# Kernel optimization log

Hardware: AMD Instinct MI355X
Metric: run time of the kernel (lower is better)

The kernel has to match this reference:

```python
import jax, jax.numpy as jnp
import numpy as np

EPS = 1e-5
GROUPS = 32
N_HEADS = 8
HEAD_DIM = 64


def setup_inputs() -> dict:
    key = jax.random.key(0)
    ks = jax.random.split(key, 8)
    b, c, d, w, hs = 2, 512, 16, 16, 16
    ctx_len, ctx_dim = 1024, 768
    inner = N_HEADS * HEAD_DIM  # 512
    return {
        "x": jax.random.normal(ks[0], (b, c, d, w, hs), jnp.float32),
        "context": jax.random.normal(ks[1], (b, ctx_len, ctx_dim), jnp.float32),
        "gamma": jnp.ones((c,), jnp.float32),
        "beta": jnp.zeros((c,), jnp.float32),
        "Wq": jax.random.normal(ks[2], (c, inner), jnp.float32) * (c ** -0.5),
        "Wk": jax.random.normal(ks[3], (ctx_dim, inner), jnp.float32) * (ctx_dim ** -0.5),
        "Wv": jax.random.normal(ks[4], (ctx_dim, inner), jnp.float32) * (ctx_dim ** -0.5),
        "Wo": jax.random.normal(ks[5], (inner, c), jnp.float32) * (inner ** -0.5),
        "bo": jnp.zeros((c,), jnp.float32),
    }


def reference(x, context, gamma, beta, Wq, Wk, Wv, Wo, bo):
    b, c, d, w, hs = x.shape
    n = d * w * hs  # sequence length of voxel tokens
    scale = HEAD_DIM ** -0.5

    # GroupNorm over (channels-in-group, spatial)
    xg = x.reshape(b, GROUPS, -1)
    mu = jnp.mean(xg, axis=-1, keepdims=True)
    var = jnp.mean(jnp.square(xg - mu), axis=-1, keepdims=True)
    xn = (xg - mu) * jax.lax.rsqrt(var + EPS)
    xn = xn.reshape(b, c, n) * gamma[None, :, None] + beta[None, :, None]

    x_seq = jnp.swapaxes(x.reshape(b, c, n), 1, 2)   # [b, n, c] residual
    xn_seq = jnp.swapaxes(xn, 1, 2)                   # [b, n, c]

    q = (xn_seq @ Wq).reshape(b, n, N_HEADS, HEAD_DIM)
    k = (context @ Wk).reshape(b, -1, N_HEADS, HEAD_DIM)
    v = (context @ Wv).reshape(b, -1, N_HEADS, HEAD_DIM)

    attn = jax.nn.softmax(jnp.einsum('bqhd,bkhd->bhqk', q, k) * scale, axis=-1)
    out = jnp.einsum('bhqk,bkhd->bqhd', attn, v).reshape(b, n, N_HEADS * HEAD_DIM)

    out = out @ Wo + bo  # dropout is identity in eval mode
    out = out + x_seq
    return jnp.swapaxes(out, 1, 2).reshape(b, c, d, w, hs)
```

## Files before the change

### kernel.cpp

```cpp
#include <hip/hip_runtime.h>
#include <hip/hip_bf16.h>

#define B 2
#define C 512
#define NTOK 4096
#define GROUPS 32
#define CPG 16
#define CTX 1024
#define CDIM 768
#define NH 8
#define HD 64
#define INNER 512
#define EPS 1e-5f
#define KVBLK 64
#define NCH (CTX / KVBLK)
#define LOG2E 1.44269504f

typedef unsigned short bf16_t;
typedef __attribute__((ext_vector_type(8))) short bf16x8;
typedef __attribute__((ext_vector_type(4))) float f32x4;

__device__ __forceinline__ bf16_t f2b(float f) {
    unsigned u = __float_as_uint(f);
    u += 0x7fffu + ((u >> 16) & 1u);
    return (bf16_t)(u >> 16);
}

__device__ __forceinline__ float4 pack8(const float* v) {
    union { ushort s[8]; float4 f; } u;
    #pragma unroll
    for (int j = 0; j < 8; ++j) u.s[j] = f2b(v[j]);
    return u.f;
}

__device__ __forceinline__ int swz(int row, int col) {
    return row * 64 + (col ^ ((row & 7) << 3));
}

__global__ __launch_bounds__(256) void gn_partial_kernel(const float* __restrict__ x,
                                                         float2* __restrict__ partials) {
    int blk = blockIdx.x;
    const float* base = x + (size_t)blk * 4096;
    float s = 0.f, ss = 0.f;
    #pragma unroll
    for (int i = 0; i < 4; ++i) {
        float4 v = *(const float4*)&base[(threadIdx.x + i * 256) * 4];
        s += v.x + v.y + v.z + v.w;
        ss += v.x * v.x + v.y * v.y + v.z * v.z + v.w * v.w;
    }
    #pragma unroll
    for (int o = 32; o > 0; o >>= 1) { s += __shfl_xor(s, o); ss += __shfl_xor(ss, o); }
    __shared__ float ls[2][4];
    int wv = threadIdx.x >> 6, ln = threadIdx.x & 63;
    if (ln == 0) { ls[0][wv] = s; ls[1][wv] = ss; }
    __syncthreads();
    if (threadIdx.x == 0) {
        partials[blk] = make_float2(ls[0][0] + ls[0][1] + ls[0][2] + ls[0][3],
                                    ls[1][0] + ls[1][1] + ls[1][2] + ls[1][3]);
    }
}

__global__ __launch_bounds__(256) void gn_apply_kernel(const float* __restrict__ x,
                                                       const float2* __restrict__ partials,
                                                       const float* __restrict__ gamma,
                                                       const float* __restrict__ beta,
                                                       bf16_t* __restrict__ xn) {
    __shared__ float tile[32][33];
    __shared__ float gmu[2], grs[2];
    int b = blockIdx.z;
    int c0 = blockIdx.y * 32;
    int t0 = blockIdx.x * 32;
    int tid = threadIdx.x;
    if (tid < 32) {
        int gi = tid >> 4, pi = tid & 15;
        float2 pp = partials[b * C + c0 + gi * 16 + pi];
        float s = pp.x, ss = pp.y;
        #pragma unroll
        for (int o = 8; o > 0; o >>= 1) { s += __shfl_xor(s, o); ss += __shfl_xor(ss, o); }
        if (pi == 0) {
            float mu = s / (float)(CPG * NTOK);
            float var = ss / (float)(CPG * NTOK) - mu * mu;
            gmu[gi] = mu;
            grs[gi] = rsqrtf(var + EPS);
        }
    }
    int tt = tid & 31, cr = tid >> 5;
    __syncthreads();
    #pragma unroll
    for (int i = 0; i < 4; ++i) {
        int co = cr + 8 * i;
        int c = c0 + co;
        float mu = gmu[co >> 4], rs = grs[co >> 4];
        float v = x[((size_t)(b * C + c)) * NTOK + t0 + tt];
        tile[co][tt] = (v - mu) * rs * gamma[c] + beta[c];
    }
    __syncthreads();
    #pragma unroll
    for (int i = 0; i < 4; ++i) {
        int t = t0 + cr + 8 * i;
        int c = c0 + tt;
        xn[((size_t)b * NTOK + t) * C + c] = f2b(tile[tt][cr + 8 * i]);
    }
}

__global__ __launch_bounds__(256) void wcast_all_kernel(
    const float* __restrict__ Wq, const float* __restrict__ Wk,
    const float* __restrict__ Wv, const float* __restrict__ Wo,
    bf16_t* __restrict__ Wqt, bf16_t* __restrict__ Wkvt, bf16_t* __restrict__ Wot) {
    int z = blockIdx.z;
    const float* in; bf16_t* out; int K;
    if (z == 0)      { in = Wq; out = Wqt;  K = C; }
    else if (z == 1) { in = Wk; out = Wkvt; K = CDIM; }
    else if (z == 2) { in = Wv; out = Wkvt + (size_t)INNER * CDIM; K = CDIM; }
    else             { in = Wo; out = Wot;  K = INNER; }
    int k0 = blockIdx.x * 32, n0 = blockIdx.y * 32;
    if (k0 >= K) return;
    __shared__ float t[32][33];
    int xx = threadIdx.x & 31, yy = threadIdx.x >> 5;
    #pragma unroll
    for (int i = 0; i < 4; ++i)
        t[yy + 8 * i][xx] = in[(size_t)(k0 + yy + 8 * i) * INNER + n0 + xx];
    __syncthreads();
    #pragma unroll
    for (int i = 0; i < 4; ++i)
        out[(size_t)(n0 + yy + 8 * i) * K + k0 + xx] = f2b(t[xx][yy + 8 * i]);
}

template <int AFP32>
__global__ __launch_bounds__(256) void gemm_qkv_kernel(
    const void* __restrict__ Av, const bf16_t* __restrict__ Bt,
    bf16_t* __restrict__ outK, bf16_t* __restrict__ outV,
    int K, int seqshift, float oscale, int vtrans) {
    __shared__ __align__(16) bf16_t As[64][40];
    __shared__ __align__(16) bf16_t Bs[64][40];
    const int tid = threadIdx.x;
    const int l = tid & 63, w = tid >> 6;
    const int wr = w >> 1, wc = w & 1;
    const int lg = l >> 4, lr = l & 15;
    const int m0 = blockIdx.x * 64, n0 = blockIdx.y * 64;
    const int rowS = tid >> 2, c8 = (tid & 3) * 8;
    const bf16_t* pa16 = AFP32 ? nullptr : (const bf16_t*)Av + (size_t)(m0 + rowS) * K + c8;
    const float*  pa32 = AFP32 ? (const float*)Av + (size_t)(m0 + rowS) * K + c8 : nullptr;
    const bf16_t* pb = Bt + (size_t)(n0 + rowS) * K + c8;
    f32x4 acc[2][2] = {};
    float av[8];
    float4 ra, rb;
    if (AFP32) {
        *(float4*)&av[0] = *(const float4*)pa32;
        *(float4*)&av[4] = *(const float4*)(pa32 + 4);
        ra = pack8(av);
    } else {
        ra = *(const float4*)pa16;
    }
    rb = *(const float4*)pb;
    *(float4*)&As[rowS][c8] = ra;
    *(float4*)&Bs[rowS][c8] = rb;
    for (int k0 = 0; k0 < K; k0 += 32) {
        __syncthreads();
        if (k0 + 32 < K) {
            if (AFP32) {
                *(float4*)&av[0] = *(const float4*)(pa32 + k0 + 32);
                *(float4*)&av[4] = *(const float4*)(pa32 + k0 + 36);
                ra = pack8(av);
            } else {
                ra = *(const float4*)(pa16 + k0 + 32);
            }
            rb = *(const float4*)(pb + k0 + 32);
        }
        bf16x8 af[2], bfm[2];
        af[0]  = *(bf16x8*)&As[wr * 32 + lr][lg * 8];
        af[1]  = *(bf16x8*)&As[wr * 32 + 16 + lr][lg * 8];
        bfm[0] = *(bf16x8*)&Bs[wc * 32 + lr][lg * 8];
        bfm[1] = *(bf16x8*)&Bs[wc * 32 + 16 + lr][lg * 8];
        #pragma unroll
        for (int mi = 0; mi < 2; ++mi)
            #pragma unroll
            for (int ni = 0; ni < 2; ++ni)
                acc[mi][ni] = __builtin_amdgcn_mfma_f32_16x16x32_bf16(af[mi], bfm[ni], acc[mi][ni], 0, 0, 0);
        __syncthreads();
        if (k0 + 32 < K) {
            *(float4*)&As[rowS][c8] = ra;
            *(float4*)&Bs[rowS][c8] = rb;
        }
    }
    const int seqmask = (1 << seqshift) - 1;
    #pragma unroll
    for (int ni = 0; ni < 2; ++ni) {
        int n = n0 + wc * 32 + ni * 16 + lr;
        int nn = n & (INNER - 1);
        int h = nn >> 6, dd = nn & 63;
        bool isV = (n >= INNER);
        #pragma unroll
        for (int mi = 0; mi < 2; ++mi) {
            int mb = m0 + wr * 32 + mi * 16 + lg * 4;
            int bidx = mb >> seqshift, seqb = mb & seqmask;
            if (isV && vtrans) {
                ushort4 pv;
                pv.x = f2b(acc[mi][ni][0] * oscale);
                pv.y = f2b(acc[mi][ni][1] * oscale);
                pv.z = f2b(acc[mi][ni][2] * oscale);
                pv.w = f2b(acc[mi][ni][3] * oscale);
                *(ushort4*)&outV[((size_t)(bidx * NH + h) * HD + dd) * (size_t)(seqmask + 1) + seqb] = pv;
            } else {
                bf16_t* dst = isV ? outV : outK;
                #pragma unroll
                for (int r = 0; r < 4; ++r)
                    dst[(((size_t)(bidx * NH + h) << seqshift) + seqb + r) * HD + dd] =
                        f2b(acc[mi][ni][r] * oscale);
            }
        }
    }
}

__global__ __launch_bounds__(256) void gemm_o_kernel(
    const bf16_t* __restrict__ A, const bf16_t* __restrict__ Bt,
    const float* __restrict__ bo, const float* __restrict__ x,
    float* __restrict__ out) {
    __shared__ __align__(16) bf16_t As[64][40];
    __shared__ __align__(16) bf16_t Bs[64][40];
    const int tid = threadIdx.x;
    const int l = tid & 63, w = tid >> 6;
    const int wr = w >> 1, wc = w & 1;
    const int lg = l >> 4, lr = l & 15;
    const int m0 = blockIdx.x * 64, n0 = blockIdx.y * 64;
    const int rowS = tid >> 2, c8 = (tid & 3) * 8;
    const bf16_t* pa = A  + (size_t)(m0 + rowS) * INNER + c8;
    const bf16_t* pb = Bt + (size_t)(n0 + rowS) * INNER + c8;
    f32x4 acc[2][2] = {};
    float4 ra = *(const float4*)pa;
    float4 rb = *(const float4*)pb;
    *(float4*)&As[rowS][c8] = ra;
    *(float4*)&Bs[rowS][c8] = rb;
    for (int k0 = 0; k0 < INNER; k0 += 32) {
        __syncthreads();
        if (k0 + 32 < INNER) {
            ra = *(const float4*)(pa + k0 + 32);
            rb = *(const float4*)(pb + k0 + 32);
        }
        bf16x8 af[2], bfm[2];
        af[0]  = *(bf16x8*)&As[wr * 32 + lr][lg * 8];
        af[1]  = *(bf16x8*)&As[wr * 32 + 16 + lr][lg * 8];
        bfm[0] = *(bf16x8*)&Bs[wc * 32 + lr][lg * 8];
        bfm[1] = *(bf16x8*)&Bs[wc * 32 + 16 + lr][lg * 8];
        #pragma unroll
        for (int mi = 0; mi < 2; ++mi)
            #pragma unroll
            for (int ni = 0; ni < 2; ++ni)
                acc[mi][ni] = __builtin_amdgcn_mfma_f32_16x16x32_bf16(af[mi], bfm[ni], acc[mi][ni], 0, 0, 0);
        __syncthreads();
        if (k0 + 32 < INNER) {
            *(float4*)&As[rowS][c8] = ra;
            *(float4*)&Bs[rowS][c8] = rb;
        }
    }
    #pragma unroll
    for (int mi = 0; mi < 2; ++mi) {
        int mb = m0 + wr * 32 + mi * 16 + lg * 4;
        int t = mb & (NTOK - 1);
        int bb = mb >> 12;
        #pragma unroll
        for (int ni = 0; ni < 2; ++ni) {
            int cc = n0 + wc * 32 + ni * 16 + lr;
            size_t o = (((size_t)(bb * C + cc)) << 12) + t;
            float4 xr = *(const float4*)&x[o];
            float bias = bo[cc];
            float4 ov;
            ov.x = acc[mi][ni][0] + bias + xr.x;
            ov.y = acc[mi][ni][1] + bias + xr.y;
            ov.z = acc[mi][ni][2] + bias + xr.z;
            ov.w = acc[mi][ni][3] + bias + xr.w;
            *(float4*)&out[o] = ov;
        }
    }
}

__global__ __launch_bounds__(256) void attn_kernel(
    const bf16_t* __restrict__ Q, const bf16_t* __restrict__ Kb,
    const bf16_t* __restrict__ Vt, bf16_t* __restrict__ AO) {
    __shared__ __align__(16) bf16_t Ks[64 * 64];
    __shared__ __align__(16) bf16_t Vs[64 * 64];
    __shared__ __align__(16) bf16_t Ps[4][16 * 64];
    const int tid = threadIdx.x;
    const int l = tid & 63, w = tid >> 6;
    const int lg = l >> 4, lr = l & 15;
    const int bh = blockIdx.x >> 6;
    const int tile = blockIdx.x & 63;
    const int b = bh >> 3, h = bh & 7;
    const int t0 = tile * 64 + w * 16;

    const bf16_t* qbase = Q + ((size_t)bh * NTOK + t0 + lr) * HD;
    bf16x8 qf[2];
    qf[0] = *(const bf16x8*)&qbase[lg * 8];
    qf[1] = *(const bf16x8*)&qbase[32 + lg * 8];

    f32x4 acc[4] = {};
    float mrow[4], lrow[4];
    #pragma unroll
    for (int r = 0; r < 4; ++r) { mrow[r] = -1e30f; lrow[r] = 0.f; }

    const bf16_t* kbase = Kb + (size_t)bh * CTX * HD;
    const bf16_t* vbase = Vt + (size_t)bh * HD * CTX;
    const int srow = tid >> 3, sc8 = (tid & 7) * 8;

    float4 kr0 = *(const float4*)&kbase[(size_t)srow * HD + sc8];
    float4 kr1 = *(const float4*)&kbase[(size_t)(srow + 32) * HD + sc8];
    float4 vr0 = *(const float4*)&vbase[(size_t)srow * CTX + sc8];
    float4 vr1 = *(const float4*)&vbase[(size_t)(srow + 32) * CTX + sc8];
    *(float4*)&Ks[swz(srow, sc8)] = kr0;
    *(float4*)&Ks[swz(srow + 32, sc8)] = kr1;
    *(float4*)&Vs[swz(srow, sc8)] = vr0;
    *(float4*)&Vs[swz(srow + 32, sc8)] = vr1;

    for (int c = 0; c < NCH; ++c) {
        __syncthreads();
        if (c + 1 < NCH) {
            int k1 = (c + 1) * KVBLK;
            kr0 = *(const float4*)&kbase[(size_t)(k1 + srow) * HD + sc8];
            kr1 = *(const float4*)&kbase[(size_t)(k1 + srow + 32) * HD + sc8];
            vr0 = *(const float4*)&vbase[(size_t)srow * CTX + k1 + sc8];
            vr1 = *(const float4*)&vbase[(size_t)(srow + 32) * CTX + k1 + sc8];
        }
        f32x4 sf[4] = {};
        #pragma unroll
        for (int ks = 0; ks < 2; ++ks)
            #pragma unroll
            for (int ni = 0; ni < 4; ++ni) {
                bf16x8 kf = *(bf16x8*)&Ks[swz(ni * 16 + lr, ks * 32 + lg * 8)];
                sf[ni] = __builtin_amdgcn_mfma_f32_16x16x32_bf16(qf[ks], kf, sf[ni], 0, 0, 0);
            }
        #pragma unroll
        for (int r = 0; r < 4; ++r) {
            float s0 = sf[0][r], s1 = sf[1][r];
            float s2 = sf[2][r], s3 = sf[3][r];
            float cm = fmaxf(fmaxf(s0, s1), fmaxf(s2, s3));
            cm = fmaxf(cm, __shfl_xor(cm, 1));
            cm = fmaxf(cm, __shfl_xor(cm, 2));
            cm = fmaxf(cm, __shfl_xor(cm, 4));
            cm = fmaxf(cm, __shfl_xor(cm, 8));
            float mn = fmaxf(mrow[r], cm);
            float scl = __builtin_amdgcn_exp2f(mrow[r] - mn);
            float p0 = __builtin_amdgcn_exp2f(s0 - mn);
            float p1 = __builtin_amdgcn_exp2f(s1 - mn);
            float p2 = __builtin_amdgcn_exp2f(s2 - mn);
            float p3 = __builtin_amdgcn_exp2f(s3 - mn);
            float rs = p0 + p1 + p2 + p3;
            rs += __shfl_xor(rs, 1); rs += __shfl_xor(rs, 2);
            rs += __shfl_xor(rs, 4); rs += __shfl_xor(rs, 8);
            lrow[r] = lrow[r] * scl + rs;
            mrow[r] = mn;
            #pragma unroll
            for (int ni = 0; ni < 4; ++ni) acc[ni][r] *= scl;
            int prow = lg * 4 + r;
            Ps[w][swz(prow, 0 * 16 + lr)] = f2b(p0);
            Ps[w][swz(prow, 1 * 16 + lr)] = f2b(p1);
            Ps[w][swz(prow, 2 * 16 + lr)] = f2b(p2);
            Ps[w][swz(prow, 3 * 16 + lr)] = f2b(p3);
        }
        #pragma unroll
        for (int ks = 0; ks < 2; ++ks) {
            bf16x8 pf = *(bf16x8*)&Ps[w][swz(lr, ks * 32 + lg * 8)];
            #pragma unroll
            for (int ni = 0; ni < 4; ++ni) {
                bf16x8 vf = *(bf16x8*)&Vs[swz(ni * 16 + lr, ks * 32 + lg * 8)];
                acc[ni] = __builtin_amdgcn_mfma_f32_16x16x32_bf16(pf, vf, acc[ni], 0, 0, 0);
            }
        }
        __syncthreads();
        if (c + 1 < NCH) {
            *(float4*)&Ks[swz(srow, sc8)] = kr0;
            *(float4*)&Ks[swz(srow + 32, sc8)] = kr1;
            *(float4*)&Vs[swz(srow, sc8)] = vr0;
            *(float4*)&Vs[swz(srow + 32, sc8)] = vr1;
        }
    }

    #pragma unroll
    for (int ni = 0; ni < 4; ++ni)
        #pragma unroll
        for (int r = 0; r < 4; ++r) {
            int t = t0 + lg * 4 + r;
            AO[((size_t)b * NTOK + t) * INNER + h * HD + ni * 16 + lr] =
                f2b(acc[ni][r] / lrow[r]);
        }
}

extern "C" void kernel_launch(void* const* d_in, const int* in_sizes, int n_in,
                              void* d_out, int out_size, void* d_ws, size_t ws_size,
                              hipStream_t stream) {
    const float* x       = (const float*)d_in[0];
    const float* context = (const float*)d_in[1];
    const float* gamma   = (const float*)d_in[2];
    const float* beta    = (const float*)d_in[3];
    const float* Wq      = (const float*)d_in[4];
    const float* Wk      = (const float*)d_in[5];
    const float* Wv      = (const float*)d_in[6];
    const float* Wo      = (const float*)d_in[7];
    const float* bo      = (const float*)d_in[8];
    float* out = (float*)d_out;

    char* p = (char*)d_ws;
    float2* parts = (float2*)p;          p += 1024 * sizeof(float2);
    bf16_t* xn   = (bf16_t*)p;           p += (size_t)B * NTOK * C * 2;
    bf16_t* Wqt  = (bf16_t*)p;           p += (size_t)INNER * C * 2;
    bf16_t* Wkvt = (bf16_t*)p;           p += (size_t)2 * INNER * CDIM * 2;
    bf16_t* Wot  = (bf16_t*)p;           p += (size_t)C * INNER * 2;
    bf16_t* qb   = (bf16_t*)p;           p += (size_t)B * NH * NTOK * HD * 2;
    bf16_t* kb   = (bf16_t*)p;           p += (size_t)B * NH * CTX * HD * 2;
    bf16_t* vb   = (bf16_t*)p;           p += (size_t)B * NH * CTX * HD * 2;
    bf16_t* ao   = (bf16_t*)p;           p += (size_t)B * NTOK * INNER * 2;

    hipLaunchKernelGGL(gn_partial_kernel, dim3(B * C), dim3(256), 0, stream, x, parts);
    hipLaunchKernelGGL(gn_apply_kernel, dim3(NTOK / 32, C / 32, B), dim3(256), 0, stream,
                       x, parts, gamma, beta, xn);
    hipLaunchKernelGGL(wcast_all_kernel, dim3(24, 16, 4), dim3(256), 0, stream,
                       Wq, Wk, Wv, Wo, Wqt, Wkvt, Wot);
    hipLaunchKernelGGL((gemm_qkv_kernel<0>), dim3(128, 8), dim3(256), 0, stream,
                       (const void*)xn, Wqt, qb, qb, C, 12, 0.125f * LOG2E, 0);
    hipLaunchKernelGGL((gemm_qkv_kernel<1>), dim3(32, 16), dim3(256), 0, stream,
                       (const void*)context, Wkvt, kb, vb, CDIM, 10, 1.0f, 1);
    hipLaunchKernelGGL(attn_kernel, dim3(B * NH * (NTOK / 64)), dim3(256), 0, stream,
                       qb, kb, vb, ao);
    hipLaunchKernelGGL(gemm_o_kernel, dim3(128, 8), dim3(256), 0, stream,
                       ao, Wot, bo, x, out);
}
```

Baseline: 194.7 us.

## Transpose QK^T MFMA so each lane owns one query row in softmax

Swaps the MFMA operands for the score computation so the result is S^T, with each lane holding 16 scores of a single query row. The row max and row sum then need only two cross-lane shuffles instead of four per row times four rows, and running max/sum become scalars per lane. P is packed with v_cvt_pk_bf16_f32 and written to LDS as 8-byte stores instead of scalar 2-byte stores. The rescale factors and final denominators are redistributed to the accumulator layout with __shfl, which adds some shuffle traffic and relies on the inline-asm conversion being available on the target.

```diff
diff --git a/kernel.cpp b/kernel.cpp
--- a/kernel.cpp
+++ b/kernel.cpp
@@ -31,6 +31,12 @@
     #pragma unroll
     for (int j = 0; j < 8; ++j) u.s[j] = f2b(v[j]);
     return u.f;
+}
+
+__device__ __forceinline__ unsigned cvtpk(float lo, float hi) {
+    unsigned r;
+    asm("v_cvt_pk_bf16_f32 %0, %1, %2" : "=v"(r) : "v"(lo), "v"(hi));
+    return r;
 }
 
 __device__ __forceinline__ int swz(int row, int col) {
@@ -294,9 +300,8 @@
     qf[1] = *(const bf16x8*)&qbase[32 + lg * 8];
 
     f32x4 acc[4] = {};
-    float mrow[4], lrow[4];
-    #pragma unroll
-    for (int r = 0; r < 4; ++r) { mrow[r] = -1e30f; lrow[r] = 0.f; }
+    float mrow = -1e30f;
+    float lrow = 0.f;
 
     const bf16_t* kbase = Kb + (size_t)bh * CTX * HD;
     const bf16_t* vbase = Vt + (size_t)bh * HD * CTX;
@@ -326,39 +331,47 @@
             #pragma unroll
             for (int ni = 0; ni < 4; ++ni) {
                 bf16x8 kf = *(bf16x8*)&Ks[swz(ni * 16 + lr, ks * 32 + lg * 8)];
-                sf[ni] = __builtin_amdgcn_mfma_f32_16x16x32_bf16(qf[ks], kf, sf[ni], 0, 0, 0);
+                sf[ni] = __builtin_amdgcn_mfma_f32_16x16x32_bf16(kf, qf[ks], sf[ni], 0, 0, 0);
             }
-        #pragma unroll
-        for (int r = 0; r < 4; ++r) {
-            float s0 = sf[0][r], s1 = sf[1][r];
-            float s2 = sf[2][r], s3 = sf[3][r];
-            float cm = fmaxf(fmaxf(s0, s1), fmaxf(s2, s3));
-            cm = fmaxf(cm, __shfl_xor(cm, 1));
-            cm = fmaxf(cm, __shfl_xor(cm, 2));
-            cm = fmaxf(cm, __shfl_xor(cm, 4));
-            cm = fmaxf(cm, __shfl_xor(cm, 8));
-            float mn = fmaxf(mrow[r], cm);
-            float scl = __builtin_amdgcn_exp2f(mrow[r] - mn);
-            float p0 = __builtin_amdgcn_exp2f(s0 - mn);
-            float p1 = __builtin_amdgcn_exp2f(s1 - mn);
-            float p2 = __builtin_amdgcn_exp2f(s2 - mn);
-            float p3 = __builtin_amdgcn_exp2f(s3 - mn);
-            float rs = p0 + p1 + p2 + p3;
-            rs += __shfl_xor(rs, 1); rs += __shfl_xor(rs, 2);
-            rs += __shfl_xor(rs, 4); rs += __shfl_xor(rs, 8);
-            lrow[r] = lrow[r] * scl + rs;
-            mrow[r] = mn;
-            #pragma unroll
-            for (int ni = 0; ni < 4; ++ni) acc[ni][r] *= scl;
-            int prow = lg * 4 + r;
-            Ps[w][swz(prow, 0 * 16 + lr)] = f2b(p0);
-            Ps[w][swz(prow, 1 * 16 + lr)] = f2b(p1);
-            Ps[w][swz(prow, 2 * 16 + lr)] = f2b(p2);
-            Ps[w][swz(prow, 3 * 16 + lr)] = f2b(p3);
-        }
+        float cm = sf[0][0];
+        #pragma unroll
+        for (int ni = 0; ni < 4; ++ni)
+            #pragma unroll
+            for (int r = 0; r < 4; ++r) cm = fmaxf(cm, sf[ni][r]);
+        cm = fmaxf(cm, __shfl_xor(cm, 16));
+        cm = fmaxf(cm, __shfl_xor(cm, 32));
+        float mn = fmaxf(mrow, cm);
+        float scl = __builtin_amdgcn_exp2f(mrow - mn);
+        mrow = mn;
+        float p[4][4];
+        float rs = 0.f;
+        #pragma unroll
+        for (int ni = 0; ni < 4; ++ni)
+            #pragma unroll
+            for (int r = 0; r < 4; ++r) {
+                p[ni][r] = __builtin_amdgcn_exp2f(sf[ni][r] - mn);
+                rs += p[ni][r];
+            }
+        rs += __shfl_xor(rs, 16);
+        rs += __shfl_xor(rs, 32);
+        lrow = lrow * scl + rs;
+        #pragma unroll
+        for (int ni = 0; ni < 4; ++ni) {
+            unsigned pk0 = cvtpk(p[ni][0], p[ni][1]);
+            unsigned pk1 = cvtpk(p[ni][2], p[ni][3]);
+            *(uint2*)&Ps[w][swz(lr, ni * 16 + 4 * lg)] = make_uint2(pk0, pk1);
+        }
+        float sclr[4];
+        #pragma unroll
+        for (int r = 0; r < 4; ++r)
+            sclr[r] = __shfl(scl, (l & 48) | (4 * lg + r));
+        #pragma unroll
+        for (int ni = 0; ni < 4; ++ni)
+            #pragma unroll
+            for (int r = 0; r < 4; ++r) acc[ni][r] *= sclr[r];
         #pragma unroll
         for (int ks = 0; ks < 2; ++ks) {
-            bf16x8 pf = *(bf16x8*)&Ps[w][swz(lr, ks * 32 + lg * 8)];
+            bf16x8 pf = *(bf16x8*)&Ps[w][swz(lr, ks * 32 + 8 * lg)];
             #pragma unroll
             for (int ni = 0; ni < 4; ++ni) {
                 bf16x8 vf = *(bf16x8*)&Vs[swz(ni * 16 + lr, ks * 32 + lg * 8)];
@@ -374,13 +387,17 @@
         }
     }
 
+    float lfin[4];
+    #pragma unroll
+    for (int r = 0; r < 4; ++r)
+        lfin[r] = __shfl(lrow, (l & 48) | (4 * lg + r));
     #pragma unroll
     for (int ni = 0; ni < 4; ++ni)
         #pragma unroll
         for (int r = 0; r < 4; ++r) {
             int t = t0 + lg * 4 + r;
             AO[((size_t)b * NTOK + t) * INNER + h * HD + ni * 16 + lr] =
-                f2b(acc[ni][r] / lrow[r]);
+                f2b(acc[ni][r] / lfin[r]);
         }
 }
 
```

Measured after the change: 171.5 us. -11.9%, faster.
